# Optimization experiments

Hardware: AMD Instinct MI355X
Metric: run time of the kernel (lower is better)

The kernel has to match this reference:

```python
import jax, jax.numpy as jnp
import numpy as np

N_NODES = 100000
N_EDGES = 1600000
N_FEAT = 64
DIM = 32
N_CLASSES = 10
N_GRAPHS = 64
BN_EPS = 1e-5


def setup_inputs() -> dict:
    key = jax.random.key(0)
    ks = jax.random.split(key, 20)
    x = jax.random.normal(ks[0], (N_NODES, N_FEAT), dtype=jnp.float32)
    edge_index = jax.random.randint(ks[1], (2, N_EDGES), 0, N_NODES, dtype=jnp.int64)
    batch = jnp.sort(jax.random.randint(ks[2], (N_NODES,), 0, N_GRAPHS, dtype=jnp.int64))
    s = 0.1
    # conv1 MLP (in=N_FEAT)
    w1a = jax.random.normal(ks[3], (N_FEAT, DIM), dtype=jnp.float32) * s
    b1a = jnp.zeros((DIM,), jnp.float32)
    w1b = jax.random.normal(ks[4], (DIM, DIM), dtype=jnp.float32) * s
    b1b = jnp.zeros((DIM,), jnp.float32)
    # convs 2-5 MLPs stacked [4, DIM, DIM]
    Wa = jax.random.normal(ks[5], (4, DIM, DIM), dtype=jnp.float32) * s
    Ba = jnp.zeros((4, DIM), jnp.float32)
    Wb = jax.random.normal(ks[6], (4, DIM, DIM), dtype=jnp.float32) * s
    Bb = jnp.zeros((4, DIM), jnp.float32)
    bn_gamma = jnp.ones((5, DIM), jnp.float32)
    bn_beta = jnp.zeros((5, DIM), jnp.float32)
    fc1_w = jax.random.normal(ks[7], (DIM, DIM), dtype=jnp.float32) * s
    fc1_b = jnp.zeros((DIM,), jnp.float32)
    fc2_w = jax.random.normal(ks[8], (DIM, N_CLASSES), dtype=jnp.float32) * s
    fc2_b = jnp.zeros((N_CLASSES,), jnp.float32)
    return dict(x=x, edge_index=edge_index, batch=batch,
                w1a=w1a, b1a=b1a, w1b=w1b, b1b=b1b,
                Wa=Wa, Ba=Ba, Wb=Wb, Bb=Bb,
                bn_gamma=bn_gamma, bn_beta=bn_beta,
                fc1_w=fc1_w, fc1_b=fc1_b, fc2_w=fc2_w, fc2_b=fc2_b)


def _gin_aggr(x, src, dst):
    # sum_{j in N(i)} x_j  + x_i   (eps = 0)
    agg = jax.ops.segment_sum(x[src], dst, num_segments=N_NODES)
    return x + agg


def _mlp(h, wa, ba, wb, bb):
    return jax.nn.relu(h @ wa + ba) @ wb + bb


def _bn(h, gamma, beta):
    mu = jnp.mean(h, axis=0)
    var = jnp.mean((h - mu) ** 2, axis=0)  # biased, torch BN training mode
    return (h - mu) * jax.lax.rsqrt(var + BN_EPS) * gamma + beta


def reference(x, edge_index, batch, w1a, b1a, w1b, b1b, Wa, Ba, Wb, Bb,
              bn_gamma, bn_beta, fc1_w, fc1_b, fc2_w, fc2_b):
    src, dst = edge_index[0], edge_index[1]
    # layer 1 (num_features -> dim)
    h = _mlp(_gin_aggr(x, src, dst), w1a, b1a, w1b, b1b)
    h = _bn(jax.nn.relu(h), bn_gamma[0], bn_beta[0])
    # layers 2-5 (dim -> dim)
    for i in range(4):
        h = _mlp(_gin_aggr(h, src, dst), Wa[i], Ba[i], Wb[i], Bb[i])
        h = _bn(jax.nn.relu(h), bn_gamma[i + 1], bn_beta[i + 1])
    # global add pool over graphs
    g = jax.ops.segment_sum(h, batch, num_segments=N_GRAPHS)  # [G, dim]
    g = jax.nn.relu(g @ fc1_w + fc1_b)
    # dropout: eval mode -> identity
    return g @ fc2_w + fc2_b  # [G, num_classes]
```

## Files before the change

### kernel.cpp

```cpp
#include <hip/hip_runtime.h>
#include <hip/hip_fp16.h>

#define NN 100000
#define NE 1600000
#define NF 64
#define DM 32
#define NG 64
#define NC 10
#define BN_EPS 1e-5f

#define BSHIFT 8
#define NBUCK ((NN + 255) >> 8)
#define CHUNK 8192
#define NCH ((NE + CHUNK - 1) / CHUNK)

__device__ __forceinline__ float2 up2(unsigned u) {
    __half2 h = __builtin_bit_cast(__half2, u);
    return __half22float2(h);
}
__device__ __forceinline__ unsigned pk2(float a, float b) {
    __half2 h = __floats2half2_rn(a, b);
    return __builtin_bit_cast(unsigned, h);
}

__global__ __launch_bounds__(256) void binA_k(const int* __restrict__ ei,
                                              int* __restrict__ bcnt) {
    __shared__ int h[NBUCK];
    for (int i = threadIdx.x; i < NBUCK; i += 256) h[i] = 0;
    __syncthreads();
    long long base = (long long)blockIdx.x * CHUNK;
    int n = (int)((NE - base < CHUNK) ? (NE - base) : CHUNK);
    for (int i = threadIdx.x; i < n; i += 256) {
        int d = ei[NE + base + i];
        atomicAdd(&h[d >> BSHIFT], 1);
    }
    __syncthreads();
    for (int i = threadIdx.x; i < NBUCK; i += 256)
        if (h[i]) atomicAdd(&bcnt[i], h[i]);
}

__global__ __launch_bounds__(512) void binB_k(const int* __restrict__ bcnt,
                                              int* __restrict__ bbase,
                                              int* __restrict__ bcur) {
    __shared__ int s[512];
    int t = threadIdx.x;
    int v = (t < NBUCK) ? bcnt[t] : 0;
    s[t] = v;
    __syncthreads();
    int acc = v;
    for (int off = 1; off < 512; off <<= 1) {
        int add = (t >= off) ? s[t - off] : 0;
        __syncthreads();
        acc += add;
        s[t] = acc;
        __syncthreads();
    }
    if (t < NBUCK) { bbase[t] = acc - v; bcur[t] = acc - v; }
    if (t == 0) bbase[NBUCK] = NE;
}

__global__ __launch_bounds__(256) void binC_k(const int* __restrict__ ei,
                                              int* __restrict__ bcur,
                                              unsigned* __restrict__ binned) {
    __shared__ int cnt[NBUCK];
    __shared__ int ofs[NBUCK];
    __shared__ int idx[NBUCK];
    for (int i = threadIdx.x; i < NBUCK; i += 256) { cnt[i] = 0; idx[i] = 0; }
    __syncthreads();
    long long base = (long long)blockIdx.x * CHUNK;
    int n = (int)((NE - base < CHUNK) ? (NE - base) : CHUNK);
    int d[CHUNK / 256];
#pragma unroll
    for (int k = 0; k < CHUNK / 256; k++) {
        int i = threadIdx.x + k * 256;
        int dd = (i < n) ? ei[NE + base + i] : -1;
        d[k] = dd;
        if (dd >= 0) atomicAdd(&cnt[dd >> BSHIFT], 1);
    }
    __syncthreads();
    for (int i = threadIdx.x; i < NBUCK; i += 256)
        if (cnt[i]) ofs[i] = atomicAdd(&bcur[i], cnt[i]);
    __syncthreads();
#pragma unroll
    for (int k = 0; k < CHUNK / 256; k++) {
        int i = threadIdx.x + k * 256;
        if (i < n) {
            unsigned src = (unsigned)ei[base + i];
            int b = d[k] >> BSHIFT;
            int l = atomicAdd(&idx[b], 1);
            binned[ofs[b] + l] = (src << 8) | (unsigned)(d[k] & 255);
        }
    }
}

__global__ __launch_bounds__(256) void binD_k(const unsigned* __restrict__ binned,
                                              const int* __restrict__ bbase,
                                              int* __restrict__ rowptr,
                                              int* __restrict__ csr) {
    __shared__ int cnt[256];
    __shared__ int cur[256];
    __shared__ int s[256];
    int b = blockIdx.x;
    int e0 = bbase[b], e1 = bbase[b + 1];
    int t = threadIdx.x;
    cnt[t] = 0;
    __syncthreads();
    for (int e = e0 + t; e < e1; e += 256) atomicAdd(&cnt[binned[e] & 255u], 1);
    __syncthreads();
    int v = cnt[t];
    s[t] = v;
    __syncthreads();
    int acc = v;
    for (int off = 1; off < 256; off <<= 1) {
        int add = (t >= off) ? s[t - off] : 0;
        __syncthreads();
        acc += add;
        s[t] = acc;
        __syncthreads();
    }
    int base = e0 + acc - v;
    int node = (b << BSHIFT) + t;
    if (node < NN) rowptr[node] = base;
    cur[t] = base;
    if (b == NBUCK - 1 && t == 0) rowptr[NN] = NE;
    __syncthreads();
    for (int e = e0 + t; e < e1; e += 256) {
        unsigned w = binned[e];
        int p = atomicAdd(&cur[w & 255u], 1);
        csr[p] = (int)(w >> 8);
    }
}

__global__ __launch_bounds__(256) void pre1_k(const float* __restrict__ x,
                                              const float* __restrict__ wa,
                                              float* __restrict__ y,
                                              unsigned* __restrict__ yhf,
                                              float* __restrict__ zbuf) {
    __shared__ float sWa[64 * 32];
    int tid = threadIdx.x;
    if (blockIdx.x == 0) {
        for (int i = tid; i < 5 * 64 + NG * 32; i += 256) zbuf[i] = 0.f;
    }
    for (int i = tid; i < 64 * 32; i += 256) sWa[i] = wa[i];
    __syncthreads();
    int node = blockIdx.x * 256 + tid;
    if (node >= NN) return;
    float t[32];
#pragma unroll
    for (int j = 0; j < 32; j++) t[j] = 0.f;
    const float4* xr = reinterpret_cast<const float4*>(x + (long long)node * 64);
    const float4* w4 = reinterpret_cast<const float4*>(sWa);
    for (int k4 = 0; k4 < 16; k4++) {
        float4 xv = xr[k4];
        int kb = k4 * 4;
#pragma unroll
        for (int q = 0; q < 8; q++) {
            float4 w0 = w4[(kb + 0) * 8 + q];
            float4 w1 = w4[(kb + 1) * 8 + q];
            float4 w2 = w4[(kb + 2) * 8 + q];
            float4 w3 = w4[(kb + 3) * 8 + q];
            t[4 * q + 0] += xv.x * w0.x + xv.y * w1.x + xv.z * w2.x + xv.w * w3.x;
            t[4 * q + 1] += xv.x * w0.y + xv.y * w1.y + xv.z * w2.y + xv.w * w3.y;
            t[4 * q + 2] += xv.x * w0.z + xv.y * w1.z + xv.z * w2.z + xv.w * w3.z;
            t[4 * q + 3] += xv.x * w0.w + xv.y * w1.w + xv.z * w2.w + xv.w * w3.w;
        }
    }
    float4* yr = reinterpret_cast<float4*>(y + (long long)node * 32);
#pragma unroll
    for (int q = 0; q < 8; q++) {
        float4 o;
        o.x = t[4 * q]; o.y = t[4 * q + 1]; o.z = t[4 * q + 2]; o.w = t[4 * q + 3];
        yr[q] = o;
    }
    uint4* yb = reinterpret_cast<uint4*>(yhf) + (long long)node * 4;
#pragma unroll
    for (int g = 0; g < 4; g++) {
        uint4 p;
        p.x = pk2(t[8 * g + 0], t[8 * g + 1]);
        p.y = pk2(t[8 * g + 2], t[8 * g + 3]);
        p.z = pk2(t[8 * g + 4], t[8 * g + 5]);
        p.w = pk2(t[8 * g + 6], t[8 * g + 7]);
        yb[g] = p;
    }
}

template <bool BN>
__global__ __launch_bounds__(256) void gatherH_k(const unsigned* __restrict__ thf,
                                                 const int* __restrict__ rowptr,
                                                 const int* __restrict__ csr,
                                                 float* __restrict__ agg,
                                                 const float* __restrict__ st,
                                                 const float* __restrict__ gamma,
                                                 const float* __restrict__ beta) {
    int tid = threadIdx.x;
    int node = blockIdx.x * 64 + (tid >> 2);
    int l = tid & 3;
    if (node >= NN) return;
    float sc[8], sh[8];
    if (BN) {
        const float invn = 1.0f / NN;
#pragma unroll
        for (int c = 0; c < 8; c++) {
            int f = 8 * l + c;
            float mu = st[f] * invn;
            float var = st[32 + f] * invn - mu * mu;
            float scale = rsqrtf(var + BN_EPS) * gamma[f];
            sc[c] = scale;
            sh[c] = beta[f] - mu * scale;
        }
    }
    int s = rowptr[node], e = rowptr[node + 1];
    const uint4* t4 = reinterpret_cast<const uint4*>(thf);
    float a[8];
#pragma unroll
    for (int c = 0; c < 8; c++) a[c] = 0.f;
    int i = s;
    for (; i + 4 <= e; i += 4) {
        int s0 = csr[i], s1 = csr[i + 1], s2 = csr[i + 2], s3 = csr[i + 3];
        uint4 w0 = t4[(long long)s0 * 4 + l];
        uint4 w1 = t4[(long long)s1 * 4 + l];
        uint4 w2 = t4[(long long)s2 * 4 + l];
        uint4 w3 = t4[(long long)s3 * 4 + l];
        float2 p;
        p = up2(w0.x); a[0] += p.x; a[1] += p.y;
        p = up2(w0.y); a[2] += p.x; a[3] += p.y;
        p = up2(w0.z); a[4] += p.x; a[5] += p.y;
        p = up2(w0.w); a[6] += p.x; a[7] += p.y;
        p = up2(w1.x); a[0] += p.x; a[1] += p.y;
        p = up2(w1.y); a[2] += p.x; a[3] += p.y;
        p = up2(w1.z); a[4] += p.x; a[5] += p.y;
        p = up2(w1.w); a[6] += p.x; a[7] += p.y;
        p = up2(w2.x); a[0] += p.x; a[1] += p.y;
        p = up2(w2.y); a[2] += p.x; a[3] += p.y;
        p = up2(w2.z); a[4] += p.x; a[5] += p.y;
        p = up2(w2.w); a[6] += p.x; a[7] += p.y;
        p = up2(w3.x); a[0] += p.x; a[1] += p.y;
        p = up2(w3.y); a[2] += p.x; a[3] += p.y;
        p = up2(w3.z); a[4] += p.x; a[5] += p.y;
        p = up2(w3.w); a[6] += p.x; a[7] += p.y;
    }
    for (; i < e; i++) {
        uint4 w = t4[(long long)csr[i] * 4 + l];
        float2 p;
        p = up2(w.x); a[0] += p.x; a[1] += p.y;
        p = up2(w.y); a[2] += p.x; a[3] += p.y;
        p = up2(w.z); a[4] += p.x; a[5] += p.y;
        p = up2(w.w); a[6] += p.x; a[7] += p.y;
    }
    if (BN) {
        float deg = (float)(e - s);
#pragma unroll
        for (int c = 0; c < 8; c++) a[c] = a[c] * sc[c] + deg * sh[c];
    }
    float4* ar = reinterpret_cast<float4*>(agg + (long long)node * 32 + l * 8);
    float4 o0, o1;
    o0.x = a[0]; o0.y = a[1]; o0.z = a[2]; o0.w = a[3];
    o1.x = a[4]; o1.y = a[5]; o1.z = a[6]; o1.w = a[7];
    ar[0] = o0;
    ar[1] = o1;
}

__global__ __launch_bounds__(256) void mlp1b_k(const float* __restrict__ y,
                                               const float* __restrict__ agg,
                                               const float* __restrict__ ba,
                                               const float* __restrict__ wb,
                                               const float* __restrict__ bb,
                                               float* __restrict__ out,
                                               unsigned* __restrict__ outhf,
                                               float* __restrict__ stats) {
    __shared__ float sWb[32 * 32];
    __shared__ float sBa[32], sBb[32];
    __shared__ float sSum[4 * 32], sSq[4 * 32];
    int tid = threadIdx.x;
    for (int i = tid; i < 32 * 32; i += 256) sWb[i] = wb[i];
    if (tid < 32) { sBa[tid] = ba[tid]; sBb[tid] = bb[tid]; }
    __syncthreads();

    int node = blockIdx.x * 256 + tid;
    float r[32];
    if (node < NN) {
        const float4* yr = reinterpret_cast<const float4*>(y + (long long)node * 32);
        const float4* ar = reinterpret_cast<const float4*>(agg + (long long)node * 32);
#pragma unroll
        for (int j = 0; j < 32; j++) r[j] = sBb[j];
        const float4* v4 = reinterpret_cast<const float4*>(sWb);
        for (int k4 = 0; k4 < 8; k4++) {
            float4 yv = yr[k4];
            float4 av = ar[k4];
            int kb = k4 * 4;
            float t0 = fmaxf(yv.x + av.x + sBa[kb + 0], 0.f);
            float t1 = fmaxf(yv.y + av.y + sBa[kb + 1], 0.f);
            float t2 = fmaxf(yv.z + av.z + sBa[kb + 2], 0.f);
            float t3 = fmaxf(yv.w + av.w + sBa[kb + 3], 0.f);
#pragma unroll
            for (int q = 0; q < 8; q++) {
                float4 w0 = v4[(kb + 0) * 8 + q];
                float4 w1 = v4[(kb + 1) * 8 + q];
                float4 w2 = v4[(kb + 2) * 8 + q];
                float4 w3 = v4[(kb + 3) * 8 + q];
                r[4 * q + 0] += t0 * w0.x + t1 * w1.x + t2 * w2.x + t3 * w3.x;
                r[4 * q + 1] += t0 * w0.y + t1 * w1.y + t2 * w2.y + t3 * w3.y;
                r[4 * q + 2] += t0 * w0.z + t1 * w1.z + t2 * w2.z + t3 * w3.z;
                r[4 * q + 3] += t0 * w0.w + t1 * w1.w + t2 * w2.w + t3 * w3.w;
            }
        }
#pragma unroll
        for (int j = 0; j < 32; j++) r[j] = fmaxf(r[j], 0.f);
        float4* orow = reinterpret_cast<float4*>(out + (long long)node * 32);
#pragma unroll
        for (int q = 0; q < 8; q++) {
            float4 o;
            o.x = r[4 * q]; o.y = r[4 * q + 1]; o.z = r[4 * q + 2]; o.w = r[4 * q + 3];
            orow[q] = o;
        }
        uint4* ob = reinterpret_cast<uint4*>(outhf) + (long long)node * 4;
#pragma unroll
        for (int g = 0; g < 4; g++) {
            uint4 p;
            p.x = pk2(r[8 * g + 0], r[8 * g + 1]);
            p.y = pk2(r[8 * g + 2], r[8 * g + 3]);
            p.z = pk2(r[8 * g + 4], r[8 * g + 5]);
            p.w = pk2(r[8 * g + 6], r[8 * g + 7]);
            ob[g] = p;
        }
    } else {
#pragma unroll
        for (int j = 0; j < 32; j++) r[j] = 0.f;
    }

    int lane = tid & 63, wid = tid >> 6;
#pragma unroll
    for (int j = 0; j < 32; j++) {
        float v = r[j], v2 = v * v;
#pragma unroll
        for (int off = 32; off >= 1; off >>= 1) {
            v += __shfl_down(v, off, 64);
            v2 += __shfl_down(v2, off, 64);
        }
        if (lane == 0) { sSum[wid * 32 + j] = v; sSq[wid * 32 + j] = v2; }
    }
    __syncthreads();
    if (tid < 32) {
        float a = sSum[tid] + sSum[32 + tid] + sSum[64 + tid] + sSum[96 + tid];
        float b = sSq[tid] + sSq[32 + tid] + sSq[64 + tid] + sSq[96 + tid];
        atomicAdd(&stats[tid], a);
        atomicAdd(&stats[32 + tid], b);
    }
}

__global__ __launch_bounds__(256) void mlp32_bn_k(float* __restrict__ h,
                                                  unsigned* __restrict__ hhf,
                                                  const float* __restrict__ agg,
                                                  const float* __restrict__ wa,
                                                  const float* __restrict__ ba,
                                                  const float* __restrict__ wb,
                                                  const float* __restrict__ bb,
                                                  const float* __restrict__ st,
                                                  const float* __restrict__ gamma,
                                                  const float* __restrict__ beta,
                                                  float* __restrict__ statsOut) {
    __shared__ float sWa[32 * 32];
    __shared__ float sWb[32 * 32];
    __shared__ float sBa[32], sBb[32];
    __shared__ float sSc[32], sSh[32];
    __shared__ float sSum[4 * 32], sSq[4 * 32];
    int tid = threadIdx.x;
    for (int i = tid; i < 32 * 32; i += 256) { sWa[i] = wa[i]; sWb[i] = wb[i]; }
    if (tid < 32) {
        sBa[tid] = ba[tid]; sBb[tid] = bb[tid];
        const float invn = 1.0f / NN;
        float mu = st[tid] * invn;
        float var = st[32 + tid] * invn - mu * mu;
        float scale = rsqrtf(var + BN_EPS) * gamma[tid];
        sSc[tid] = scale;
        sSh[tid] = beta[tid] - mu * scale;
    }
    __syncthreads();

    int node = blockIdx.x * 256 + tid;
    float r[32];
    if (node < NN) {
        float t[32];
#pragma unroll
        for (int j = 0; j < 32; j++) t[j] = sBa[j];
        const float4* hr = reinterpret_cast<const float4*>(h + (long long)node * 32);
        const float4* ar = reinterpret_cast<const float4*>(agg + (long long)node * 32);
        const float4* w4 = reinterpret_cast<const float4*>(sWa);
        for (int k4 = 0; k4 < 8; k4++) {
            float4 xv = hr[k4];
            float4 av = ar[k4];
            int kb = k4 * 4;
            float a0 = xv.x * sSc[kb + 0] + sSh[kb + 0] + av.x;
            float a1 = xv.y * sSc[kb + 1] + sSh[kb + 1] + av.y;
            float a2 = xv.z * sSc[kb + 2] + sSh[kb + 2] + av.z;
            float a3 = xv.w * sSc[kb + 3] + sSh[kb + 3] + av.w;
#pragma unroll
            for (int q = 0; q < 8; q++) {
                float4 w0 = w4[(kb + 0) * 8 + q];
                float4 w1 = w4[(kb + 1) * 8 + q];
                float4 w2 = w4[(kb + 2) * 8 + q];
                float4 w3 = w4[(kb + 3) * 8 + q];
                t[4 * q + 0] += a0 * w0.x + a1 * w1.x + a2 * w2.x + a3 * w3.x;
                t[4 * q + 1] += a0 * w0.y + a1 * w1.y + a2 * w2.y + a3 * w3.y;
                t[4 * q + 2] += a0 * w0.z + a1 * w1.z + a2 * w2.z + a3 * w3.z;
                t[4 * q + 3] += a0 * w0.w + a1 * w1.w + a2 * w2.w + a3 * w3.w;
            }
        }
#pragma unroll
        for (int j = 0; j < 32; j++) t[j] = fmaxf(t[j], 0.f);
#pragma unroll
        for (int j = 0; j < 32; j++) r[j] = sBb[j];
        const float4* v4 = reinterpret_cast<const float4*>(sWb);
        for (int k = 0; k < 32; k++) {
            float a = t[k];
#pragma unroll
            for (int q = 0; q < 8; q++) {
                float4 w = v4[k * 8 + q];
                r[4 * q + 0] += a * w.x;
                r[4 * q + 1] += a * w.y;
                r[4 * q + 2] += a * w.z;
                r[4 * q + 3] += a * w.w;
            }
        }
#pragma unroll
        for (int j = 0; j < 32; j++) r[j] = fmaxf(r[j], 0.f);
        float4* orow = reinterpret_cast<float4*>(h + (long long)node * 32);
#pragma unroll
        for (int q = 0; q < 8; q++) {
            float4 o;
            o.x = r[4 * q]; o.y = r[4 * q + 1]; o.z = r[4 * q + 2]; o.w = r[4 * q + 3];
            orow[q] = o;
        }
        uint4* ob = reinterpret_cast<uint4*>(hhf) + (long long)node * 4;
#pragma unroll
        for (int g = 0; g < 4; g++) {
            uint4 p;
            p.x = pk2(r[8 * g + 0], r[8 * g + 1]);
            p.y = pk2(r[8 * g + 2], r[8 * g + 3]);
            p.z = pk2(r[8 * g + 4], r[8 * g + 5]);
            p.w = pk2(r[8 * g + 6], r[8 * g + 7]);
            ob[g] = p;
        }
    } else {
#pragma unroll
        for (int j = 0; j < 32; j++) r[j] = 0.f;
    }

    int lane = tid & 63, wid = tid >> 6;
#pragma unroll
    for (int j = 0; j < 32; j++) {
        float v = r[j], v2 = v * v;
#pragma unroll
        for (int off = 32; off >= 1; off >>= 1) {
            v += __shfl_down(v, off, 64);
            v2 += __shfl_down(v2, off, 64);
        }
        if (lane == 0) { sSum[wid * 32 + j] = v; sSq[wid * 32 + j] = v2; }
    }
    __syncthreads();
    if (tid < 32) {
        float a = sSum[tid] + sSum[32 + tid] + sSum[64 + tid] + sSum[96 + tid];
        float b = sSq[tid] + sSq[32 + tid] + sSq[64 + tid] + sSq[96 + tid];
        atomicAdd(&statsOut[tid], a);
        atomicAdd(&statsOut[32 + tid], b);
    }
}

#define POOL_NPB 512
__global__ __launch_bounds__(256) void pool_bn_k(const float* __restrict__ h,
                                                 const int* __restrict__ batch,
                                                 const float* __restrict__ st,
                                                 const float* __restrict__ gamma,
                                                 const float* __restrict__ beta,
                                                 float* __restrict__ pooled) {
    int tid = threadIdx.x;
    int f = tid & 31;
    int p = tid >> 5;
    int n0 = blockIdx.x * POOL_NPB + p * (POOL_NPB / 8);
    int n1 = n0 + POOL_NPB / 8;
    if (n1 > NN) n1 = NN;
    if (n0 >= NN) return;
    const float invn = 1.0f / NN;
    float mu = st[f] * invn;
    float var = st[32 + f] * invn - mu * mu;
    float sc = rsqrtf(var + BN_EPS) * gamma[f];
    float sh = beta[f] - mu * sc;
    float acc = 0.f;
    int cur = batch[n0];
    for (int n = n0; n < n1; n++) {
        int g = batch[n];
        if (g != cur) {
            atomicAdd(&pooled[cur * 32 + f], acc);
            cur = g;
            acc = 0.f;
        }
        acc += h[(long long)n * 32 + f] * sc + sh;
    }
    atomicAdd(&pooled[cur * 32 + f], acc);
}

__global__ __launch_bounds__(64) void final_k(const float* __restrict__ pooled,
                                              const float* __restrict__ w1,
                                              const float* __restrict__ b1,
                                              const float* __restrict__ w2,
                                              const float* __restrict__ b2,
                                              float* __restrict__ out) {
    int g = threadIdx.x;
    if (g >= NG) return;
    float t[32];
#pragma unroll
    for (int j = 0; j < 32; j++) t[j] = b1[j];
    for (int k = 0; k < 32; k++) {
        float a = pooled[g * 32 + k];
#pragma unroll
        for (int j = 0; j < 32; j++) t[j] += a * w1[k * 32 + j];
    }
#pragma unroll
    for (int j = 0; j < 32; j++) t[j] = fmaxf(t[j], 0.f);
    for (int c = 0; c < NC; c++) {
        float o = b2[c];
#pragma unroll
        for (int k = 0; k < 32; k++) o += t[k] * w2[k * NC + c];
        out[g * NC + c] = o;
    }
}

extern "C" void kernel_launch(void* const* d_in, const int* in_sizes, int n_in,
                              void* d_out, int out_size, void* d_ws, size_t ws_size,
                              hipStream_t stream) {
    const float* x = (const float*)d_in[0];
    const int* ei = (const int*)d_in[1];
    const int* batch = (const int*)d_in[2];
    const float* w1a = (const float*)d_in[3];
    const float* b1a = (const float*)d_in[4];
    const float* w1b = (const float*)d_in[5];
    const float* b1b = (const float*)d_in[6];
    const float* Wa = (const float*)d_in[7];
    const float* Ba = (const float*)d_in[8];
    const float* Wb = (const float*)d_in[9];
    const float* Bb = (const float*)d_in[10];
    const float* bn_gamma = (const float*)d_in[11];
    const float* bn_beta = (const float*)d_in[12];
    const float* fc1w = (const float*)d_in[13];
    const float* fc1b = (const float*)d_in[14];
    const float* fc2w = (const float*)d_in[15];
    const float* fc2b = (const float*)d_in[16];
    float* out = (float*)d_out;

    float* ws = (float*)d_ws;
    float* y = ws;
    float* hb = y + (size_t)NN * 32;
    float* agg = hb + (size_t)NN * 32;
    float* stats_all = agg + (size_t)NN * 32;
    float* pooled = stats_all + 5 * 64;
    unsigned* yhf = (unsigned*)(pooled + NG * 32);
    unsigned* hbhf = yhf + (size_t)NN * 16;
    unsigned* binned = hbhf + (size_t)NN * 16;
    int* bcnt = (int*)(binned + NE);
    int* bbase = bcnt + NBUCK;
    int* bcur = bbase + NBUCK + 1;
    int* rowptr = bcur + NBUCK;
    int* csr = rowptr + NN + 1;

    const int nodeBlocks = (NN + 255) / 256;
    const int gBlocks = (NN + 63) / 64;

    hipMemsetAsync(bcnt, 0, NBUCK * sizeof(int), stream);
    binA_k<<<NCH, 256, 0, stream>>>(ei, bcnt);
    binB_k<<<1, 512, 0, stream>>>(bcnt, bbase, bcur);
    binC_k<<<NCH, 256, 0, stream>>>(ei, bcur, binned);
    binD_k<<<NBUCK, 256, 0, stream>>>(binned, bbase, rowptr, csr);

    pre1_k<<<nodeBlocks, 256, 0, stream>>>(x, w1a, y, yhf, stats_all);
    gatherH_k<false><<<gBlocks, 256, 0, stream>>>(yhf, rowptr, csr, agg,
                                                  nullptr, nullptr, nullptr);
    mlp1b_k<<<nodeBlocks, 256, 0, stream>>>(y, agg, b1a, w1b, b1b, hb, hbhf, stats_all);

    for (int i = 0; i < 4; i++) {
        const float* st = stats_all + i * 64;
        const float* g = bn_gamma + i * 32;
        const float* be = bn_beta + i * 32;
        gatherH_k<true><<<gBlocks, 256, 0, stream>>>(hbhf, rowptr, csr, agg, st, g, be);
        mlp32_bn_k<<<nodeBlocks, 256, 0, stream>>>(hb, hbhf, agg, Wa + i * 1024, Ba + i * 32,
                                                   Wb + i * 1024, Bb + i * 32,
                                                   st, g, be, stats_all + (i + 1) * 64);
    }

    pool_bn_k<<<(NN + POOL_NPB - 1) / POOL_NPB, 256, 0, stream>>>(
        hb, batch, stats_all + 4 * 64, bn_gamma + 4 * 32, bn_beta + 4 * 32, pooled);
    final_k<<<1, 64, 0, stream>>>(pooled, fc1w, fc1b, fc2w, fc2b, out);
}
```

Measured before the change: 504.5 us.

## Split per-node MLP work across four lanes per node

The dense per-node MLP kernels (pre1, mlp1b, mlp32_bn) now assign four threads to each node instead of one. Each thread computes eight output features, and intermediate activations are exchanged between the four lanes with shuffles. This cuts per-thread register pressure from 32-wide accumulators to 8 and launches four times as many blocks, aiming for higher occupancy and more coalesced row accesses. In exchange it adds shuffle traffic and redundant per-thread input reads in mlp32_bn, where each lane still loads the full 32-wide input row.

After: 584.0 us. +15.8%, slower.

```diff
diff --git a/kernel.cpp b/kernel.cpp
--- a/kernel.cpp
+++ b/kernel.cpp
@@ -143,45 +143,36 @@
     }
     for (int i = tid; i < 64 * 32; i += 256) sWa[i] = wa[i];
     __syncthreads();
-    int node = blockIdx.x * 256 + tid;
+    int l = tid & 3;
+    int node = blockIdx.x * 64 + (tid >> 2);
     if (node >= NN) return;
-    float t[32];
-#pragma unroll
-    for (int j = 0; j < 32; j++) t[j] = 0.f;
+    float t[8];
+#pragma unroll
+    for (int j = 0; j < 8; j++) t[j] = 0.f;
     const float4* xr = reinterpret_cast<const float4*>(x + (long long)node * 64);
     const float4* w4 = reinterpret_cast<const float4*>(sWa);
+#pragma unroll
     for (int k4 = 0; k4 < 16; k4++) {
         float4 xv = xr[k4];
-        int kb = k4 * 4;
-#pragma unroll
-        for (int q = 0; q < 8; q++) {
-            float4 w0 = w4[(kb + 0) * 8 + q];
-            float4 w1 = w4[(kb + 1) * 8 + q];
-            float4 w2 = w4[(kb + 2) * 8 + q];
-            float4 w3 = w4[(kb + 3) * 8 + q];
-            t[4 * q + 0] += xv.x * w0.x + xv.y * w1.x + xv.z * w2.x + xv.w * w3.x;
-            t[4 * q + 1] += xv.x * w0.y + xv.y * w1.y + xv.z * w2.y + xv.w * w3.y;
-            t[4 * q + 2] += xv.x * w0.z + xv.y * w1.z + xv.z * w2.z + xv.w * w3.z;
-            t[4 * q + 3] += xv.x * w0.w + xv.y * w1.w + xv.z * w2.w + xv.w * w3.w;
+        float av[4] = {xv.x, xv.y, xv.z, xv.w};
+#pragma unroll
+        for (int i = 0; i < 4; i++) {
+            float a = av[i];
+            float4 w0 = w4[(k4 * 4 + i) * 8 + 2 * l];
+            float4 w1 = w4[(k4 * 4 + i) * 8 + 2 * l + 1];
+            t[0] += a * w0.x; t[1] += a * w0.y; t[2] += a * w0.z; t[3] += a * w0.w;
+            t[4] += a * w1.x; t[5] += a * w1.y; t[6] += a * w1.z; t[7] += a * w1.w;
         }
     }
-    float4* yr = reinterpret_cast<float4*>(y + (long long)node * 32);
-#pragma unroll
-    for (int q = 0; q < 8; q++) {
-        float4 o;
-        o.x = t[4 * q]; o.y = t[4 * q + 1]; o.z = t[4 * q + 2]; o.w = t[4 * q + 3];
-        yr[q] = o;
-    }
-    uint4* yb = reinterpret_cast<uint4*>(yhf) + (long long)node * 4;
-#pragma unroll
-    for (int g = 0; g < 4; g++) {
-        uint4 p;
-        p.x = pk2(t[8 * g + 0], t[8 * g + 1]);
-        p.y = pk2(t[8 * g + 2], t[8 * g + 3]);
-        p.z = pk2(t[8 * g + 4], t[8 * g + 5]);
-        p.w = pk2(t[8 * g + 6], t[8 * g + 7]);
-        yb[g] = p;
-    }
+    float4* yr = reinterpret_cast<float4*>(y + (long long)node * 32 + l * 8);
+    float4 o0, o1;
+    o0.x = t[0]; o0.y = t[1]; o0.z = t[2]; o0.w = t[3];
+    o1.x = t[4]; o1.y = t[5]; o1.z = t[6]; o1.w = t[7];
+    yr[0] = o0; yr[1] = o1;
+    uint4 p;
+    p.x = pk2(t[0], t[1]); p.y = pk2(t[2], t[3]);
+    p.z = pk2(t[4], t[5]); p.w = pk2(t[6], t[7]);
+    reinterpret_cast<uint4*>(yhf)[(long long)node * 4 + l] = p;
 }
 
 template <bool BN>
@@ -276,68 +267,66 @@
     if (tid < 32) { sBa[tid] = ba[tid]; sBb[tid] = bb[tid]; }
     __syncthreads();
 
-    int node = blockIdx.x * 256 + tid;
-    float r[32];
-    if (node < NN) {
-        const float4* yr = reinterpret_cast<const float4*>(y + (long long)node * 32);
-        const float4* ar = reinterpret_cast<const float4*>(agg + (long long)node * 32);
-#pragma unroll
-        for (int j = 0; j < 32; j++) r[j] = sBb[j];
-        const float4* v4 = reinterpret_cast<const float4*>(sWb);
-        for (int k4 = 0; k4 < 8; k4++) {
-            float4 yv = yr[k4];
-            float4 av = ar[k4];
-            int kb = k4 * 4;
-            float t0 = fmaxf(yv.x + av.x + sBa[kb + 0], 0.f);
-            float t1 = fmaxf(yv.y + av.y + sBa[kb + 1], 0.f);
-            float t2 = fmaxf(yv.z + av.z + sBa[kb + 2], 0.f);
-            float t3 = fmaxf(yv.w + av.w + sBa[kb + 3], 0.f);
-#pragma unroll
-            for (int q = 0; q < 8; q++) {
-                float4 w0 = v4[(kb + 0) * 8 + q];
-                float4 w1 = v4[(kb + 1) * 8 + q];
-                float4 w2 = v4[(kb + 2) * 8 + q];
-                float4 w3 = v4[(kb + 3) * 8 + q];
-                r[4 * q + 0] += t0 * w0.x + t1 * w1.x + t2 * w2.x + t3 * w3.x;
-                r[4 * q + 1] += t0 * w0.y + t1 * w1.y + t2 * w2.y + t3 * w3.y;
-                r[4 * q + 2] += t0 * w0.z + t1 * w1.z + t2 * w2.z + t3 * w3.z;
-                r[4 * q + 3] += t0 * w0.w + t1 * w1.w + t2 * w2.w + t3 * w3.w;
-            }
-        }
-#pragma unroll
-        for (int j = 0; j < 32; j++) r[j] = fmaxf(r[j], 0.f);
-        float4* orow = reinterpret_cast<float4*>(out + (long long)node * 32);
-#pragma unroll
-        for (int q = 0; q < 8; q++) {
-            float4 o;
-            o.x = r[4 * q]; o.y = r[4 * q + 1]; o.z = r[4 * q + 2]; o.w = r[4 * q + 3];
-            orow[q] = o;
-        }
-        uint4* ob = reinterpret_cast<uint4*>(outhf) + (long long)node * 4;
-#pragma unroll
-        for (int g = 0; g < 4; g++) {
-            uint4 p;
-            p.x = pk2(r[8 * g + 0], r[8 * g + 1]);
-            p.y = pk2(r[8 * g + 2], r[8 * g + 3]);
-            p.z = pk2(r[8 * g + 4], r[8 * g + 5]);
-            p.w = pk2(r[8 * g + 6], r[8 * g + 7]);
-            ob[g] = p;
-        }
+    int l = tid & 3;
+    int node = blockIdx.x * 64 + (tid >> 2);
+    bool act = node < NN;
+    float t[8];
+    if (act) {
+        const float4* yr = reinterpret_cast<const float4*>(y + (long long)node * 32 + l * 8);
+        const float4* ar = reinterpret_cast<const float4*>(agg + (long long)node * 32 + l * 8);
+        float4 y0 = yr[0], y1 = yr[1], a0 = ar[0], a1 = ar[1];
+        t[0] = fmaxf(y0.x + a0.x + sBa[l * 8 + 0], 0.f);
+        t[1] = fmaxf(y0.y + a0.y + sBa[l * 8 + 1], 0.f);
+        t[2] = fmaxf(y0.z + a0.z + sBa[l * 8 + 2], 0.f);
+        t[3] = fmaxf(y0.w + a0.w + sBa[l * 8 + 3], 0.f);
+        t[4] = fmaxf(y1.x + a1.x + sBa[l * 8 + 4], 0.f);
+        t[5] = fmaxf(y1.y + a1.y + sBa[l * 8 + 5], 0.f);
+        t[6] = fmaxf(y1.z + a1.z + sBa[l * 8 + 6], 0.f);
+        t[7] = fmaxf(y1.w + a1.w + sBa[l * 8 + 7], 0.f);
     } else {
 #pragma unroll
-        for (int j = 0; j < 32; j++) r[j] = 0.f;
+        for (int j = 0; j < 8; j++) t[j] = 0.f;
+    }
+
+    float r[8];
+#pragma unroll
+    for (int j = 0; j < 8; j++) r[j] = sBb[l * 8 + j];
+    const float4* v4 = reinterpret_cast<const float4*>(sWb);
+#pragma unroll
+    for (int k = 0; k < 32; k++) {
+        float a = __shfl(t[k & 7], k >> 3, 4);
+        float4 w0 = v4[k * 8 + 2 * l];
+        float4 w1 = v4[k * 8 + 2 * l + 1];
+        r[0] += a * w0.x; r[1] += a * w0.y; r[2] += a * w0.z; r[3] += a * w0.w;
+        r[4] += a * w1.x; r[5] += a * w1.y; r[6] += a * w1.z; r[7] += a * w1.w;
+    }
+#pragma unroll
+    for (int j = 0; j < 8; j++) r[j] = fmaxf(r[j], 0.f);
+
+    if (act) {
+        float4* orow = reinterpret_cast<float4*>(out + (long long)node * 32 + l * 8);
+        float4 o0, o1;
+        o0.x = r[0]; o0.y = r[1]; o0.z = r[2]; o0.w = r[3];
+        o1.x = r[4]; o1.y = r[5]; o1.z = r[6]; o1.w = r[7];
+        orow[0] = o0; orow[1] = o1;
+        uint4 p;
+        p.x = pk2(r[0], r[1]); p.y = pk2(r[2], r[3]);
+        p.z = pk2(r[4], r[5]); p.w = pk2(r[6], r[7]);
+        reinterpret_cast<uint4*>(outhf)[(long long)node * 4 + l] = p;
+    } else {
+#pragma unroll
+        for (int j = 0; j < 8; j++) r[j] = 0.f;
     }
 
     int lane = tid & 63, wid = tid >> 6;
 #pragma unroll
-    for (int j = 0; j < 32; j++) {
+    for (int j = 0; j < 8; j++) {
         float v = r[j], v2 = v * v;
-#pragma unroll
-        for (int off = 32; off >= 1; off >>= 1) {
-            v += __shfl_down(v, off, 64);
-            v2 += __shfl_down(v2, off, 64);
-        }
-        if (lane == 0) { sSum[wid * 32 + j] = v; sSq[wid * 32 + j] = v2; }
+        v += __shfl_down(v, 32, 64); v2 += __shfl_down(v2, 32, 64);
+        v += __shfl_down(v, 16, 64); v2 += __shfl_down(v2, 16, 64);
+        v += __shfl_down(v, 8, 64);  v2 += __shfl_down(v2, 8, 64);
+        v += __shfl_down(v, 4, 64);  v2 += __shfl_down(v2, 4, 64);
+        if (lane < 4) { sSum[wid * 32 + lane * 8 + j] = v; sSq[wid * 32 + lane * 8 + j] = v2; }
     }
     __syncthreads();
     if (tid < 32) {
@@ -377,85 +366,80 @@
     }
     __syncthreads();
 
-    int node = blockIdx.x * 256 + tid;
-    float r[32];
-    if (node < NN) {
-        float t[32];
-#pragma unroll
-        for (int j = 0; j < 32; j++) t[j] = sBa[j];
+    int l = tid & 3;
+    int node = blockIdx.x * 64 + (tid >> 2);
+    bool act = node < NN;
+    float t[8];
+    const float4* w4a = reinterpret_cast<const float4*>(sWa);
+    if (act) {
+        float a[32];
         const float4* hr = reinterpret_cast<const float4*>(h + (long long)node * 32);
         const float4* ar = reinterpret_cast<const float4*>(agg + (long long)node * 32);
-        const float4* w4 = reinterpret_cast<const float4*>(sWa);
+#pragma unroll
         for (int k4 = 0; k4 < 8; k4++) {
             float4 xv = hr[k4];
             float4 av = ar[k4];
-            int kb = k4 * 4;
-            float a0 = xv.x * sSc[kb + 0] + sSh[kb + 0] + av.x;
-            float a1 = xv.y * sSc[kb + 1] + sSh[kb + 1] + av.y;
-            float a2 = xv.z * sSc[kb + 2] + sSh[kb + 2] + av.z;
-            float a3 = xv.w * sSc[kb + 3] + sSh[kb + 3] + av.w;
-#pragma unroll
-            for (int q = 0; q < 8; q++) {
-                float4 w0 = w4[(kb + 0) * 8 + q];
-                float4 w1 = w4[(kb + 1) * 8 + q];
-                float4 w2 = w4[(kb + 2) * 8 + q];
-                float4 w3 = w4[(kb + 3) * 8 + q];
-                t[4 * q + 0] += a0 * w0.x + a1 * w1.x + a2 * w2.x + a3 * w3.x;
-                t[4 * q + 1] += a0 * w0.y + a1 * w1.y + a2 * w2.y + a3 * w3.y;
-                t[4 * q + 2] += a0 * w0.z + a1 * w1.z + a2 * w2.z + a3 * w3.z;
-                t[4 * q + 3] += a0 * w0.w + a1 * w1.w + a2 * w2.w + a3 * w3.w;
-            }
+            a[k4 * 4 + 0] = xv.x * sSc[k4 * 4 + 0] + sSh[k4 * 4 + 0] + av.x;
+            a[k4 * 4 + 1] = xv.y * sSc[k4 * 4 + 1] + sSh[k4 * 4 + 1] + av.y;
+            a[k4 * 4 + 2] = xv.z * sSc[k4 * 4 + 2] + sSh[k4 * 4 + 2] + av.z;
+            a[k4 * 4 + 3] = xv.w * sSc[k4 * 4 + 3] + sSh[k4 * 4 + 3] + av.w;
         }
 #pragma unroll
-        for (int j = 0; j < 32; j++) t[j] = fmaxf(t[j], 0.f);
-#pragma unroll
-        for (int j = 0; j < 32; j++) r[j] = sBb[j];
-        const float4* v4 = reinterpret_cast<const float4*>(sWb);
+        for (int j = 0; j < 8; j++) t[j] = sBa[l * 8 + j];
+#pragma unroll
         for (int k = 0; k < 32; k++) {
-            float a = t[k];
-#pragma unroll
-            for (int q = 0; q < 8; q++) {
-                float4 w = v4[k * 8 + q];
-                r[4 * q + 0] += a * w.x;
-                r[4 * q + 1] += a * w.y;
-                r[4 * q + 2] += a * w.z;
-                r[4 * q + 3] += a * w.w;
-            }
+            float av = a[k];
+            float4 w0 = w4a[k * 8 + 2 * l];
+            float4 w1 = w4a[k * 8 + 2 * l + 1];
+            t[0] += av * w0.x; t[1] += av * w0.y; t[2] += av * w0.z; t[3] += av * w0.w;
+            t[4] += av * w1.x; t[5] += av * w1.y; t[6] += av * w1.z; t[7] += av * w1.w;
         }
 #pragma unroll
-        for (int j = 0; j < 32; j++) r[j] = fmaxf(r[j], 0.f);
-        float4* orow = reinterpret_cast<float4*>(h + (long long)node * 32);
-#pragma unroll
-        for (int q = 0; q < 8; q++) {
-            float4 o;
-            o.x = r[4 * q]; o.y = r[4 * q + 1]; o.z = r[4 * q + 2]; o.w = r[4 * q + 3];
-            orow[q] = o;
-        }
-        uint4* ob = reinterpret_cast<uint4*>(hhf) + (long long)node * 4;
-#pragma unroll
-        for (int g = 0; g < 4; g++) {
-            uint4 p;
-            p.x = pk2(r[8 * g + 0], r[8 * g + 1]);
-            p.y = pk2(r[8 * g + 2], r[8 * g + 3]);
-            p.z = pk2(r[8 * g + 4], r[8 * g + 5]);
-            p.w = pk2(r[8 * g + 6], r[8 * g + 7]);
-            ob[g] = p;
-        }
+        for (int j = 0; j < 8; j++) t[j] = fmaxf(t[j], 0.f);
     } else {
 #pragma unroll
-        for (int j = 0; j < 32; j++) r[j] = 0.f;
+        for (int j = 0; j < 8; j++) t[j] = 0.f;
+    }
+
+    float r[8];
+#pragma unroll
+    for (int j = 0; j < 8; j++) r[j] = sBb[l * 8 + j];
+    const float4* v4 = reinterpret_cast<const float4*>(sWb);
+#pragma unroll
+    for (int k = 0; k < 32; k++) {
+        float a = __shfl(t[k & 7], k >> 3, 4);
+        float4 w0 = v4[k * 8 + 2 * l];
+        float4 w1 = v4[k * 8 + 2 * l + 1];
+        r[0] += a * w0.x; r[1] += a * w0.y; r[2] += a * w0.z; r[3] += a * w0.w;
+        r[4] += a * w1.x; r[5] += a * w1.y; r[6] += a * w1.z; r[7] += a * w1.w;
+    }
+#pragma unroll
+    for (int j = 0; j < 8; j++) r[j] = fmaxf(r[j], 0.f);
+
+    if (act) {
+        float4* orow = reinterpret_cast<float4*>(h + (long long)node * 32 + l * 8);
+        float4 o0, o1;
+        o0.x = r[0]; o0.y = r[1]; o0.z = r[2]; o0.w = r[3];
+        o1.x = r[4]; o1.y = r[5]; o1.z = r[6]; o1.w = r[7];
+        orow[0] = o0; orow[1] = o1;
+        uint4 p;
+        p.x = pk2(r[0], r[1]); p.y = pk2(r[2], r[3]);
+        p.z = pk2(r[4], r[5]); p.w = pk2(r[6], r[7]);
+        reinterpret_cast<uint4*>(hhf)[(long long)node * 4 + l] = p;
+    } else {
+#pragma unroll
+        for (int j = 0; j < 8; j++) r[j] = 0.f;
     }
 
     int lane = tid & 63, wid = tid >> 6;
 #pragma unroll
-    for (int j = 0; j < 32; j++) {
+    for (int j = 0; j < 8; j++) {
         float v = r[j], v2 = v * v;
-#pragma unroll
-        for (int off = 32; off >= 1; off >>= 1) {
-            v += __shfl_down(v, off, 64);
-            v2 += __shfl_down(v2, off, 64);
-        }
-        if (lane == 0) { sSum[wid * 32 + j] = v; sSq[wid * 32 + j] = v2; }
+        v += __shfl_down(v, 32, 64); v2 += __shfl_down(v2, 32, 64);
+        v += __shfl_down(v, 16, 64); v2 += __shfl_down(v2, 16, 64);
+        v += __shfl_down(v, 8, 64);  v2 += __shfl_down(v2, 8, 64);
+        v += __shfl_down(v, 4, 64);  v2 += __shfl_down(v2, 4, 64);
+        if (lane < 4) { sSum[wid * 32 + lane * 8 + j] = v; sSq[wid * 32 + lane * 8 + j] = v2; }
     }
     __syncthreads();
     if (tid < 32) {
@@ -562,8 +546,7 @@
     int* rowptr = bcur + NBUCK;
     int* csr = rowptr + NN + 1;
 
-    const int nodeBlocks = (NN + 255) / 256;
-    const int gBlocks = (NN + 63) / 64;
+    const int nb4 = (NN + 63) / 64;
 
     hipMemsetAsync(bcnt, 0, NBUCK * sizeof(int), stream);
     binA_k<<<NCH, 256, 0, stream>>>(ei, bcnt);
@@ -571,19 +554,19 @@
     binC_k<<<NCH, 256, 0, stream>>>(ei, bcur, binned);
     binD_k<<<NBUCK, 256, 0, stream>>>(binned, bbase, rowptr, csr);
 
-    pre1_k<<<nodeBlocks, 256, 0, stream>>>(x, w1a, y, yhf, stats_all);
-    gatherH_k<false><<<gBlocks, 256, 0, stream>>>(yhf, rowptr, csr, agg,
-                                                  nullptr, nullptr, nullptr);
-    mlp1b_k<<<nodeBlocks, 256, 0, stream>>>(y, agg, b1a, w1b, b1b, hb, hbhf, stats_all);
+    pre1_k<<<nb4, 256, 0, stream>>>(x, w1a, y, yhf, stats_all);
+    gatherH_k<false><<<nb4, 256, 0, stream>>>(yhf, rowptr, csr, agg,
+                                              nullptr, nullptr, nullptr);
+    mlp1b_k<<<nb4, 256, 0, stream>>>(y, agg, b1a, w1b, b1b, hb, hbhf, stats_all);
 
     for (int i = 0; i < 4; i++) {
         const float* st = stats_all + i * 64;
         const float* g = bn_gamma + i * 32;
         const float* be = bn_beta + i * 32;
-        gatherH_k<true><<<gBlocks, 256, 0, stream>>>(hbhf, rowptr, csr, agg, st, g, be);
-        mlp32_bn_k<<<nodeBlocks, 256, 0, stream>>>(hb, hbhf, agg, Wa + i * 1024, Ba + i * 32,
-                                                   Wb + i * 1024, Bb + i * 32,
-                                                   st, g, be, stats_all + (i + 1) * 64);
+        gatherH_k<true><<<nb4, 256, 0, stream>>>(hbhf, rowptr, csr, agg, st, g, be);
+        mlp32_bn_k<<<nb4, 256, 0, stream>>>(hb, hbhf, agg, Wa + i * 1024, Ba + i * 32,
+                                            Wb + i * 1024, Bb + i * 32,
+                                            st, g, be, stats_all + (i + 1) * 64);
     }
 
     pool_bn_k<<<(NN + POOL_NPB - 1) / POOL_NPB, 256, 0, stream>>>(
```
